# Performance work log

Measured on AMD Instinct MI355X. Metric: run time of the kernel, lower is better.

Reference implementation:

```python
import jax, jax.numpy as jnp
import numpy as np

B, N, D, EPG = 64, 1024, 128, 8192          # graphs, nodes/graph, feat dim, edges/graph
NTOT, ETOT = B * N, B * EPG
RATIO, LAMB, NEG = 0.8, 1.0, 0.2
K = int(np.ceil(RATIO * N))                  # 820 kept nodes per graph (static)


def setup_inputs() -> dict:
    key = jax.random.key(0)
    k1, k2, k3, k4, k5, k6 = jax.random.split(key, 6)
    feat = jax.random.normal(k1, (NTOT, D), jnp.float32)
    offs = (jnp.arange(B, dtype=jnp.int32) * N)[:, None]
    src = (jax.random.randint(k2, (B, EPG), 0, N, jnp.int32) + offs).reshape(-1)
    dst = (jax.random.randint(k3, (B, EPG), 0, N, jnp.int32) + offs).reshape(-1)
    e_feat = jnp.ones((ETOT,), jnp.float32)  # default e_feat=None -> ones
    # xavier-normal-ish params
    W = jax.random.normal(k4, (D, D), jnp.float32) * (2.0 / (D + D)) ** 0.5
    a = jax.random.normal(k5, (D, 1), jnp.float32) * (2.0 / (D + 1)) ** 0.5
    att = jax.random.normal(k6, (1, 2 * D), jnp.float32) * (2.0 / (1 + 2 * D)) ** 0.5
    return {"feat": feat, "e_feat": e_feat, "W": W, "a": a, "att": att,
            "src": src, "dst": dst}


def sparsemax(z, axis):
    """Dense sparsemax along `axis` (shift-invariant, same as edge_sparsemax
    per destination-node group after max subtraction)."""
    n = z.shape[axis]
    zs = -jnp.sort(-z, axis=axis)                      # descending
    cs = jnp.cumsum(zs, axis=axis)
    shp = [1] * z.ndim
    shp[axis] = n
    r = jnp.arange(1, n + 1, dtype=z.dtype).reshape(shp)
    supp = (1.0 + r * zs) > cs
    kz = supp.sum(axis=axis, keepdims=True)            # support size
    tau = (jnp.take_along_axis(cs, kz - 1, axis=axis) - 1.0) / kz.astype(z.dtype)
    return jnp.clip(z - tau, 0.0)


def reference(feat, e_feat, W, a, att, src, dst):
    # ---- NodeInfoScoreLayer (sym_norm=True) ----
    ones_e = jnp.ones_like(e_feat)
    out_deg = jax.ops.segment_sum(ones_e, src, NTOT)   # degrees incl. self loops
    in_deg = jax.ops.segment_sum(ones_e, dst, NTOT)
    sn = jnp.maximum(out_deg, 1.0) ** -0.5
    dn = jnp.maximum(in_deg, 1.0) ** -0.5
    nonself = (src != dst).astype(feat.dtype)          # remove_self_loop
    msg = (feat * sn[:, None])[src] * (e_feat * nonself)[:, None]   # u_mul_e
    agg = jax.ops.segment_sum(msg, dst, NTOT)                        # sum -> h
    info = jnp.abs(feat - agg * dn[:, None]).sum(axis=1)

    # ---- node attention gate ----
    attn = jax.nn.sigmoid(jax.nn.leaky_relu((feat @ W) @ a, 0.2).squeeze(-1))
    x_score = info * attn

    # ---- per-graph top-k (equal graph sizes -> static k) ----
    _, idx = jax.lax.top_k(x_score.reshape(B, N), K)
    perm = (idx + jnp.arange(B, dtype=idx.dtype)[:, None] * N).reshape(-1)
    feat_p = feat[perm]                                # [B*K, D]

    # ---- structure learning, sample=False path: per-graph dense blocks ----
    maskarr = jnp.full((NTOT,), -1, jnp.int32).at[perm].set(
        jnp.arange(B * K, dtype=jnp.int32))
    nr, nc = maskarr[src], maskarr[dst]
    valid = (nr >= 0) & (nc >= 0)                      # edges of pooled subgraph
    nr0 = jnp.where(valid, nr, 0)
    nc0 = jnp.where(valid, nc, 0)
    bb, ii, jj = nr0 // K, nr0 % K, nc0 % K            # block-diagonal coords

    fp = feat_p.reshape(B, K, D)
    wsrc = fp @ att[0, :D]                             # [B, K]
    wdst = fp @ att[0, D:]
    Wblk = jax.nn.leaky_relu(wsrc[:, :, None] + wdst[:, None, :], NEG)  # [B,K,K]
    Wblk = Wblk.at[bb, ii, jj].add(jnp.where(valid, LAMB * e_feat, 0.0))

    # edge_sparsemax: normalize over incoming edges of each dst node
    weights = sparsemax(Wblk, axis=1)                  # over src axis
    weights = jnp.where(jnp.abs(weights) > 1e-9, weights, 0.0)

    return feat_p, weights, perm, x_score
```

## Files before the change

kernel.cpp:

```cpp
#include <hip/hip_runtime.h>
#include <math.h>


static constexpr int B_    = 64;
static constexpr int N_    = 1024;
static constexpr int D_    = 128;
static constexpr int NTOT_ = B_ * N_;
static constexpr int ETOT_ = B_ * 8192;
static constexpr int K_    = 820;
static constexpr int BK_   = B_ * K_;
static constexpr float NEG_ = 0.2f;
static constexpr int CH_   = 128;
static constexpr int CPB_  = 7;
static constexpr int CAP_  = 64;
static constexpr int NSA_  = (NTOT_ + 2047) / 2048;
static constexpr int NSB_  = (BK_ + 2047) / 2048;
static constexpr int SFLAG = 0x40000000;

typedef float fvec4 __attribute__((ext_vector_type(4)));

__device__ __forceinline__ float lrelu(float x) { return x >= 0.f ? x : NEG_ * x; }

__global__ void k_deg_wa(const int* __restrict__ src, const int* __restrict__ dst,
                         int* __restrict__ outd, int* __restrict__ ind,
                         const float* __restrict__ W, const float* __restrict__ a,
                         float* __restrict__ waf) {
  int blk = blockIdx.x;
  if (blk < ETOT_ / 256) {
    int e = blk * 256 + threadIdx.x;
    atomicAdd(&outd[src[e]], 1);
    atomicAdd(&ind[dst[e]], 1);
  } else {
    int q = blk - ETOT_ / 256;
    int w = threadIdx.x >> 6, lane = threadIdx.x & 63;
    int wid = q * 4 + w;
    double a0 = (double)a[2 * lane], a1 = (double)a[2 * lane + 1];
#pragma unroll
    for (int r = 0; r < 4; ++r) {
      int d = wid * 4 + r;
      double s = (double)W[d * D_ + 2 * lane] * a0
               + (double)W[d * D_ + 2 * lane + 1] * a1;
#pragma unroll
      for (int off = 32; off > 0; off >>= 1) s += __shfl_down(s, off);
      if (lane == 0) waf[d] = (float)s;
    }
  }
}

__device__ __forceinline__ void scan2048(const int* __restrict__ in, int n, int blk,
                                         int nblk, int* __restrict__ partials,
                                         int* __restrict__ out) {
  int t = threadIdx.x;
  int w = t >> 6, lane = t & 63;
  int base = blk * 2048 + t * 4;
  int a0 = (base < n) ? in[base] : 0;
  int a1 = (base + 1 < n) ? in[base + 1] : 0;
  int a2 = (base + 2 < n) ? in[base + 2] : 0;
  int a3 = (base + 3 < n) ? in[base + 3] : 0;
  int s = a0 + a1 + a2 + a3;
  int inc = s;
#pragma unroll
  for (int off = 1; off < 64; off <<= 1) {
    int v = __shfl_up(inc, off);
    if (lane >= off) inc += v;
  }
  __shared__ int wtot[8];
  __shared__ int sbase;
  if (lane == 63) wtot[w] = inc;
  __syncthreads();
  if (t == 0) {
    int btot = 0;
#pragma unroll
    for (int q2 = 0; q2 < 8; ++q2) btot += wtot[q2];
    __hip_atomic_store(&partials[blk], btot | SFLAG, __ATOMIC_RELEASE,
                       __HIP_MEMORY_SCOPE_AGENT);
  }
  if (t < 64) {
    int v = 0;
    if (t < blk) {
      do {
        v = __hip_atomic_load(&partials[t], __ATOMIC_ACQUIRE,
                              __HIP_MEMORY_SCOPE_AGENT);
      } while (!(v & SFLAG));
      v &= ~SFLAG;
    }
#pragma unroll
    for (int off = 32; off > 0; off >>= 1) v += __shfl_down(v, off);
    if (t == 0) sbase = v;
  }
  __syncthreads();
  int wbase = 0;
  for (int q2 = 0; q2 < w; ++q2) wbase += wtot[q2];
  int ex = sbase + wbase + inc - s;
  if (base < n) out[base] = ex; ex += a0;
  if (base + 1 < n) out[base + 1] = ex; ex += a1;
  if (base + 2 < n) out[base + 2] = ex; ex += a2;
  if (base + 3 < n) out[base + 3] = ex; ex += a3;
  if (blk == nblk - 1 && t == 511) out[n] = ex;
}

__global__ void k_scanA(const int* __restrict__ in, int* __restrict__ partials,
                        int* __restrict__ out) {
  scan2048(in, NTOT_, blockIdx.x, NSA_, partials, out);
}

__global__ void k_fillcsr(const int* __restrict__ dst, const int* __restrict__ rowptr,
                          int* __restrict__ cursor, int* __restrict__ col) {
  int e = blockIdx.x * 256 + threadIdx.x;
  int v = dst[e];
  int p = atomicAdd(&cursor[v], 1);
  col[rowptr[v] + p] = e;
}

__global__ void k_agg(const float* __restrict__ feat, const float* __restrict__ e_feat,
                      const int* __restrict__ src, const int* __restrict__ col,
                      const int* __restrict__ rowptr, const int* __restrict__ outd,
                      const int* __restrict__ ind, const float* __restrict__ waf,
                      float* __restrict__ out_xs) {
  __shared__ int su[4][CAP_];
  __shared__ float ssc[4][CAP_];
  int g = blockIdx.x;
  int vb = (g & 7) * 2048 + (g >> 3);
  int w = threadIdx.x >> 6, lane = threadIdx.x & 63;
  int v = vb * 4 + w;
  int r0 = rowptr[v], r1 = rowptr[v + 1];
  int m = r1 - r0;
  int mm = m < CAP_ ? m : CAP_;
  for (int s = lane; s < mm; s += 64) {
    int e = col[r0 + s];
    int u = src[e];
    float sc = (u == v) ? 0.f : e_feat[e] / sqrtf(fmaxf((float)outd[u], 1.f));
    su[w][s] = u;
    ssc[w][s] = sc;
  }
  __syncthreads();
  const float2* f2 = (const float2*)feat;
  float2 f = f2[(size_t)v * 64 + lane];
  float ax = 0.f, ay = 0.f;
  int s = 0;
  for (; s + 4 <= mm; s += 4) {
    int u0 = su[w][s], u1 = su[w][s + 1], u2 = su[w][s + 2], u3 = su[w][s + 3];
    float c0 = ssc[w][s], c1 = ssc[w][s + 1], c2 = ssc[w][s + 2], c3 = ssc[w][s + 3];
    float2 f0 = f2[(size_t)u0 * 64 + lane];
    float2 f1 = f2[(size_t)u1 * 64 + lane];
    float2 fq = f2[(size_t)u2 * 64 + lane];
    float2 f3 = f2[(size_t)u3 * 64 + lane];
    ax += f0.x * c0 + f1.x * c1 + fq.x * c2 + f3.x * c3;
    ay += f0.y * c0 + f1.y * c1 + fq.y * c2 + f3.y * c3;
  }
  for (; s < mm; ++s) {
    float2 fu = f2[(size_t)su[w][s] * 64 + lane];
    ax += fu.x * ssc[w][s];
    ay += fu.y * ssc[w][s];
  }
  for (int sP = r0 + CAP_; sP < r1; ++sP) {
    int e = col[sP];
    int u = src[e];
    if (u == v) continue;
    float sc = e_feat[e] / sqrtf(fmaxf((float)outd[u], 1.f));
    float2 fu = f2[(size_t)u * 64 + lane];
    ax += fu.x * sc;
    ay += fu.y * sc;
  }
  float dn = 1.f / sqrtf(fmaxf((float)ind[v], 1.f));
  float info = fabsf(f.x - ax * dn) + fabsf(f.y - ay * dn);
  float dot = f.x * waf[2 * lane] + f.y * waf[2 * lane + 1];
#pragma unroll
  for (int off = 32; off > 0; off >>= 1) {
    info += __shfl_down(info, off);
    dot  += __shfl_down(dot, off);
  }
  if (lane == 0) {
    float sA = dot >= 0.f ? dot : 0.2f * dot;
    float attn = 1.f / (1.f + expf(-sA));
    out_xs[v] = info * attn;
  }
}

__global__ void k_topk(const float* __restrict__ xs, float* __restrict__ out_perm,
                       int* __restrict__ perm_i, int* __restrict__ maskarr) {
  __shared__ unsigned long long dv[1024];
  int b = blockIdx.x, t = threadIdx.x;
  for (int i = t; i < 1024; i += 512) {
    unsigned bits = __float_as_uint(xs[b * 1024 + i]);
    dv[i] = ((unsigned long long)bits << 32) | (unsigned)(N_ - 1 - i);
  }
  __syncthreads();
  for (int k2 = 2; k2 <= 1024; k2 <<= 1) {
    for (int j = k2 >> 1; j > 0; j >>= 1) {
      for (int i = t; i < 1024; i += 512) {
        int ixj = i ^ j;
        if (ixj > i) {
          unsigned long long a = dv[i], c = dv[ixj];
          bool dir = ((i & k2) == 0);
          if ((a > c) != dir) { dv[i] = c; dv[ixj] = a; }
        }
      }
      __syncthreads();
    }
  }
  for (int r = t; r < K_; r += 512) {
    int idx = N_ - 1 - (int)(dv[r] & 0xFFFFFFFFull);
    int node = b * N_ + idx;
    int pos = b * K_ + r;
    out_perm[pos] = (float)node;
    perm_i[pos] = node;
    maskarr[node] = pos;
  }
}

__global__ void k_gather_cnt2(const float* __restrict__ feat, const int* __restrict__ perm_i,
                              const float* __restrict__ att, float* __restrict__ out_featp,
                              float* __restrict__ wsrc, float* __restrict__ wdst,
                              const int* __restrict__ src, const int* __restrict__ dst,
                              const int* __restrict__ maskarr, int* __restrict__ cnt2) {
  int blk = blockIdx.x;
  if (blk < BK_ / 4) {
    int vb = (blk & 7) * 1640 + (blk >> 3);
    int gid = vb * 256 + threadIdx.x;
    int p = gid >> 6, lane = gid & 63;
    int node = perm_i[p];
    float2 f = ((const float2*)feat)[(size_t)node * 64 + lane];
    ((float2*)out_featp)[(size_t)p * 64 + lane] = f;
    float s1 = f.x * att[2 * lane] + f.y * att[2 * lane + 1];
    float s2 = f.x * att[D_ + 2 * lane] + f.y * att[D_ + 2 * lane + 1];
#pragma unroll
    for (int off = 32; off > 0; off >>= 1) {
      s1 += __shfl_down(s1, off);
      s2 += __shfl_down(s2, off);
    }
    if (lane == 0) { wsrc[p] = s1; wdst[p] = s2; }
  } else {
    int e = (blk - BK_ / 4) * 256 + threadIdx.x;
    int nr = maskarr[src[e]], nc = maskarr[dst[e]];
    if (nr >= 0 && nc >= 0) atomicAdd(&cnt2[nc], 1);
  }
}

__global__ void k_scanB_gsort(const int* __restrict__ cnt2, int* __restrict__ partials,
                              int* __restrict__ rowptr2, const float* __restrict__ wsrc,
                              float* __restrict__ ws_sorted, float* __restrict__ psum) {
  if (blockIdx.x < NSB_) {
    scan2048(cnt2, BK_, blockIdx.x, NSB_, partials, rowptr2);
    return;
  }
  __shared__ float sv[1024];
  __shared__ float sc[1024];
  int b = blockIdx.x - NSB_, t = threadIdx.x;
  for (int i = t; i < 1024; i += 512) sv[i] = (i < K_) ? wsrc[b * K_ + i] : -INFINITY;
  __syncthreads();
  for (int k2 = 2; k2 <= 1024; k2 <<= 1) {
    for (int j = k2 >> 1; j > 0; j >>= 1) {
      for (int i = t; i < 1024; i += 512) {
        int ixj = i ^ j;
        if (ixj > i) {
          float a = sv[i], c = sv[ixj];
          bool dir = ((i & k2) == 0);
          bool swapv = dir ? (c > a) : (a > c);
          if (swapv) { sv[i] = c; sv[ixj] = a; }
        }
      }
      __syncthreads();
    }
  }
  for (int i = t; i < 1024; i += 512) { ws_sorted[b * 1024 + i] = sv[i]; sc[i] = sv[i]; }
  __syncthreads();
  for (int off = 1; off < 1024; off <<= 1) {
    float tmp[2];
    for (int i = t, q = 0; i < 1024; i += 512, ++q) tmp[q] = (i >= off) ? sc[i - off] : 0.f;
    __syncthreads();
    for (int i = t, q = 0; i < 1024; i += 512, ++q) sc[i] += tmp[q];
    __syncthreads();
  }
  if (t == 0) psum[b * 1025] = 0.f;
  for (int i = t; i < 1024; i += 512) psum[b * 1025 + 1 + i] = sc[i];
}

__global__ void k_fill2(const int* __restrict__ src, const int* __restrict__ dst,
                        const int* __restrict__ maskarr, const float* __restrict__ e_feat,
                        const int* __restrict__ rowptr2, int* __restrict__ cursor2,
                        int* __restrict__ colii, float* __restrict__ colval) {
  int e = blockIdx.x * 256 + threadIdx.x;
  int nr = maskarr[src[e]], nc = maskarr[dst[e]];
  if (nr >= 0 && nc >= 0) {
    int p = atomicAdd(&cursor2[nc], 1);
    int s = rowptr2[nc] + p;
    colii[s] = nr;
    colval[s] = 1.0f * e_feat[e];
  }
}

__device__ __forceinline__ int cnt_gt_rng(const float* __restrict__ arr, float thr,
                                          int lo, int hi) {
  while (lo < hi) {
    int mid = (lo + hi) >> 1;
    if (arr[mid] > thr) lo = mid + 1; else hi = mid;
  }
  return lo;
}

__global__ void __launch_bounds__(128) k_tau(
    const float* __restrict__ wdst,
    const float* __restrict__ ws_sorted, const float* __restrict__ psum,
    const int* __restrict__ rowptr2, int* __restrict__ ucnt,
    int* __restrict__ colii, float* __restrict__ colval,
    const float* __restrict__ wsrc, float2* __restrict__ bval,
    float* __restrict__ tauv) {
  __shared__ float swss[1024];
  __shared__ float sps[1025];
  int b = blockIdx.x / CPB_;
  int chunk = blockIdx.x % CPB_;
  int t0 = threadIdx.x;
  for (int i = t0; i < 1024; i += 128) swss[i] = ws_sorted[b * 1024 + i];
  for (int i = t0; i < 1025; i += 128) sps[i] = psum[b * 1025 + i];
  __syncthreads();

  int j = chunk * CH_ + t0;
  if (j >= K_) return;
  int c = b * K_ + j;

  int r0 = rowptr2[c], r1 = rowptr2[c + 1];
  int wp = r0;
  for (int s = r0; s < r1; ++s) {
    int ii = colii[s];
    if (ii < 0) continue;
    float E = colval[s];
    for (int t2 = s + 1; t2 < r1; ++t2)
      if (colii[t2] == ii) { E += colval[t2]; colii[t2] = -1; }
    colii[wp] = ii; colval[wp] = E; ++wp;
  }
  int m = wp - r0;
  ucnt[c] = m;
  for (int s = r0; s < wp; ++s) bval[s] = make_float2(wsrc[colii[s]], colval[s]);

  float wd = wdst[c];
  int p = cnt_gt_rng(swss, -wd, 0, K_);
  float psp = sps[p];

  float mz = lrelu(swss[0] + wd);
  for (int s = 0; s < m; ++s) {
    float2 v = bval[r0 + s];
    mz = fmaxf(mz, lrelu(v.x + wd) + v.y);
  }

  float lo = mz - 1.0f, hi = mz;
  int nmin = 0, nmax = K_;
  for (int it = 0; it < 22; ++it) {
    float t = 0.5f * (lo + hi);
    float wthr = (t >= 0.f ? t : 5.f * t) - wd;
    int n = cnt_gt_rng(swss, wthr, nmin, nmax);
    float bsum = (n <= p) ? (sps[n] + n * wd)
                          : (psp + p * wd + NEG_ * (sps[n] - psp + (n - p) * wd));
    float g = bsum - n * t;
    for (int s = 0; s < m; ++s) {
      float2 v = bval[r0 + s];
      float bse = lrelu(v.x + wd);
      g += fmaxf(bse + v.y - t, 0.f) - fmaxf(bse - t, 0.f);
    }
    if (g > 1.f) { lo = t; nmax = n; } else { hi = t; nmin = n; }
  }
  float t = lo;
  float wthr = (t >= 0.f ? t : 5.f * t) - wd;
  int n = cnt_gt_rng(swss, wthr, nmin, nmax);
  float S = (n <= p) ? (sps[n] + n * wd)
                     : (psp + p * wd + NEG_ * (sps[n] - psp + (n - p) * wd));
  int cc = n;
  for (int s = 0; s < m; ++s) {
    float2 v = bval[r0 + s];
    float bse = lrelu(v.x + wd);
    float zz = bse + v.y;
    if (v.x > wthr) { S -= bse; cc -= 1; }
    if (zz > t)     { S += zz;  cc += 1; }
  }
  float tau = (cc < 1) ? (mz - 1.0f) : ((S - 1.0f) / (float)cc);
  tau = fminf(fmaxf(tau, mz - 1.0f), mz);
  tauv[c] = tau;
}

__global__ void k_dense4(const float* __restrict__ wsrc, const float* __restrict__ wdst,
                         const float* __restrict__ tauv, float* __restrict__ out_w) {
  int t = threadIdx.x;
  int j4 = t * 4;
  if (j4 >= K_) return;
  int r0 = blockIdx.x * 4;
  int b = r0 / K_;
  float4 wd = ((const float4*)(wdst + b * K_))[t];
  float4 ta = ((const float4*)(tauv + b * K_))[t];
  float4 ws4 = ((const float4*)wsrc)[blockIdx.x];
  const float wss[4] = {ws4.x, ws4.y, ws4.z, ws4.w};
#pragma unroll
  for (int q = 0; q < 4; ++q) {
    float ws = wss[q];
    fvec4 o;
    float z;
    z = lrelu(ws + wd.x) - ta.x; o.x = (z > 1e-9f) ? z : 0.f;
    z = lrelu(ws + wd.y) - ta.y; o.y = (z > 1e-9f) ? z : 0.f;
    z = lrelu(ws + wd.z) - ta.z; o.z = (z > 1e-9f) ? z : 0.f;
    z = lrelu(ws + wd.w) - ta.w; o.w = (z > 1e-9f) ? z : 0.f;
    __builtin_nontemporal_store(o, ((fvec4*)(out_w + (size_t)(r0 + q) * K_)) + t);
  }
}

__global__ void k_fix(const float* __restrict__ wsrc, const float* __restrict__ wdst,
                      const float* __restrict__ tauv, const int* __restrict__ rowptr2,
                      const int* __restrict__ ucnt, const int* __restrict__ colii,
                      const float* __restrict__ colval, float* __restrict__ out_w) {
  int c = blockIdx.x * 256 + threadIdx.x;
  int b = c / K_;
  int j = c - b * K_;
  float wd = wdst[c], ta = tauv[c];
  int r0 = rowptr2[c], m = ucnt[c];
  for (int s = 0; s < m; ++s) {
    int nr = colii[r0 + s];
    float z = lrelu(wsrc[nr] + wd) + colval[r0 + s];
    float v = z - ta;
    out_w[(size_t)nr * K_ + j] = (v > 1e-9f) ? v : 0.f;
  }
}

extern "C" void kernel_launch(void* const* d_in, const int* in_sizes, int n_in,
                              void* d_out, int out_size, void* d_ws, size_t ws_size,
                              hipStream_t stream) {
  const float* feat   = (const float*)d_in[0];
  const float* e_feat = (const float*)d_in[1];
  const float* W      = (const float*)d_in[2];
  const float* a      = (const float*)d_in[3];
  const float* att    = (const float*)d_in[4];
  const int*   src    = (const int*)d_in[5];
  const int*   dst    = (const int*)d_in[6];

  float* out_featp = (float*)d_out;
  float* out_w     = out_featp + (size_t)BK_ * D_;
  float* out_perm  = out_w + (size_t)BK_ * K_;
  float* out_xs    = out_perm + BK_;

  char* wsp = (char*)d_ws;
  auto carve = [&](size_t bytes) -> void* {
    void* pp = (void*)wsp;
    wsp += (bytes + 255) & ~(size_t)255;
    return pp;
  };
  float* waf       = (float*)carve((size_t)D_ * 4);
  float* wsrc      = (float*)carve((size_t)BK_ * 4);
  float* wdst      = (float*)carve((size_t)BK_ * 4);
  float* tauv      = (float*)carve((size_t)BK_ * 4);
  float* colval    = (float*)carve((size_t)ETOT_ * 4);
  float2* bval     = (float2*)carve((size_t)ETOT_ * 8);
  float* ws_sorted = (float*)carve((size_t)B_ * 1024 * 4);
  float* psum      = (float*)carve((size_t)B_ * 1025 * 4);
  int* rowptr      = (int*)carve((size_t)(NTOT_ + 1) * 4);
  int* rowptr2     = (int*)carve((size_t)(BK_ + 1) * 4);
  int* col         = (int*)carve((size_t)ETOT_ * 4);
  int* colii       = (int*)carve((size_t)ETOT_ * 4);
  int* perm_i      = (int*)carve((size_t)BK_ * 4);
  size_t zbytes    = ((size_t)NTOT_ * 3 + (size_t)BK_ * 2 + 64) * 4;
  int* zblk        = (int*)carve(zbytes);
  int* in_deg      = zblk;
  int* out_deg     = zblk + NTOT_;
  int* cursor      = zblk + 2 * NTOT_;
  int* cnt2        = zblk + 3 * NTOT_;
  int* cursor2     = cnt2 + BK_;
  int* partA       = cursor2 + BK_;
  int* partB       = partA + 32;
  int* maskarr     = (int*)carve((size_t)NTOT_ * 4);

  hipMemsetAsync(zblk, 0, zbytes, stream);
  hipMemsetAsync(maskarr, 0xFF, (size_t)NTOT_ * 4, stream);

  k_deg_wa<<<ETOT_ / 256 + 8, 256, 0, stream>>>(src, dst, out_deg, in_deg, W, a, waf);
  k_scanA<<<NSA_, 512, 0, stream>>>(in_deg, partA, rowptr);
  k_fillcsr<<<ETOT_ / 256, 256, 0, stream>>>(dst, rowptr, cursor, col);
  k_agg<<<NTOT_ / 4, 256, 0, stream>>>(feat, e_feat, src, col, rowptr, out_deg, in_deg,
                                       waf, out_xs);
  k_topk<<<B_, 512, 0, stream>>>(out_xs, out_perm, perm_i, maskarr);
  k_gather_cnt2<<<BK_ / 4 + ETOT_ / 256, 256, 0, stream>>>(
      feat, perm_i, att, out_featp, wsrc, wdst, src, dst, maskarr, cnt2);
  k_scanB_gsort<<<NSB_ + B_, 512, 0, stream>>>(cnt2, partB, rowptr2, wsrc,
                                               ws_sorted, psum);
  k_fill2<<<ETOT_ / 256, 256, 0, stream>>>(src, dst, maskarr, e_feat, rowptr2, cursor2,
                                           colii, colval);
  k_tau<<<B_ * CPB_, 128, 0, stream>>>(wdst, ws_sorted, psum, rowptr2, cursor2,
                                       colii, colval, wsrc, bval, tauv);
  k_dense4<<<BK_ / 4, 256, 0, stream>>>(wsrc, wdst, tauv, out_w);
  k_fix<<<BK_ / 256, 256, 0, stream>>>(wsrc, wdst, tauv, rowptr2, cursor2, colii, colval,
                                       out_w);
}
```

Before: 539.8 us.

## Fuse all stages into one cooperative persistent kernel with grid syncs

Replaces the chain of eleven kernel launches with a single cooperative kernel of 1024 blocks. Stages are separated by grid.sync() and each stage's work is strided across the fixed grid. This removes per-launch overhead and the gaps between kernels. In exchange, stages that need few blocks (top-k, the sorts) leave most of the grid idle while waiting at barriers. Block sizes also shrink from 512 to 256 threads in the sort and scan stages, which serialises more work per thread.

```diff
diff --git a/kernel.cpp b/kernel.cpp
--- a/kernel.cpp
+++ b/kernel.cpp
@@ -1,5 +1,8 @@
 #include <hip/hip_runtime.h>
+#include <hip/hip_cooperative_groups.h>
 #include <math.h>
+
+namespace cg = cooperative_groups;
 
 
 static constexpr int B_    = 64;
@@ -10,68 +13,46 @@
 static constexpr int K_    = 820;
 static constexpr int BK_   = B_ * K_;
 static constexpr float NEG_ = 0.2f;
-static constexpr int CH_   = 128;
-static constexpr int CPB_  = 7;
 static constexpr int CAP_  = 64;
 static constexpr int NSA_  = (NTOT_ + 2047) / 2048;
 static constexpr int NSB_  = (BK_ + 2047) / 2048;
 static constexpr int SFLAG = 0x40000000;
+static constexpr int GRID_ = 1024;
 
 typedef float fvec4 __attribute__((ext_vector_type(4)));
 
 __device__ __forceinline__ float lrelu(float x) { return x >= 0.f ? x : NEG_ * x; }
 
-__global__ void k_deg_wa(const int* __restrict__ src, const int* __restrict__ dst,
-                         int* __restrict__ outd, int* __restrict__ ind,
-                         const float* __restrict__ W, const float* __restrict__ a,
-                         float* __restrict__ waf) {
-  int blk = blockIdx.x;
-  if (blk < ETOT_ / 256) {
-    int e = blk * 256 + threadIdx.x;
-    atomicAdd(&outd[src[e]], 1);
-    atomicAdd(&ind[dst[e]], 1);
-  } else {
-    int q = blk - ETOT_ / 256;
-    int w = threadIdx.x >> 6, lane = threadIdx.x & 63;
-    int wid = q * 4 + w;
-    double a0 = (double)a[2 * lane], a1 = (double)a[2 * lane + 1];
-#pragma unroll
-    for (int r = 0; r < 4; ++r) {
-      int d = wid * 4 + r;
-      double s = (double)W[d * D_ + 2 * lane] * a0
-               + (double)W[d * D_ + 2 * lane + 1] * a1;
-#pragma unroll
-      for (int off = 32; off > 0; off >>= 1) s += __shfl_down(s, off);
-      if (lane == 0) waf[d] = (float)s;
-    }
-  }
+__device__ __forceinline__ int cnt_gt_rng(const float* __restrict__ arr, float thr,
+                                          int lo, int hi) {
+  while (lo < hi) {
+    int mid = (lo + hi) >> 1;
+    if (arr[mid] > thr) lo = mid + 1; else hi = mid;
+  }
+  return lo;
 }
 
-__device__ __forceinline__ void scan2048(const int* __restrict__ in, int n, int blk,
-                                         int nblk, int* __restrict__ partials,
-                                         int* __restrict__ out) {
-  int t = threadIdx.x;
-  int w = t >> 6, lane = t & 63;
-  int base = blk * 2048 + t * 4;
-  int a0 = (base < n) ? in[base] : 0;
-  int a1 = (base + 1 < n) ? in[base + 1] : 0;
-  int a2 = (base + 2 < n) ? in[base + 2] : 0;
-  int a3 = (base + 3 < n) ? in[base + 3] : 0;
-  int s = a0 + a1 + a2 + a3;
+__device__ __forceinline__ void scan2048c(const int* __restrict__ in, int n, int blk,
+                                          int nblk, int* __restrict__ partials,
+                                          int* __restrict__ out,
+                                          unsigned char* smem_) {
+  int t = threadIdx.x, w = t >> 6, lane = t & 63;
+  int* wtot = (int*)smem_;
+  int* sbasep = (int*)(smem_ + 16);
+  int base = blk * 2048 + t * 8;
+  int a[8], s = 0;
+#pragma unroll
+  for (int q = 0; q < 8; ++q) { a[q] = (base + q < n) ? in[base + q] : 0; s += a[q]; }
   int inc = s;
 #pragma unroll
   for (int off = 1; off < 64; off <<= 1) {
     int v = __shfl_up(inc, off);
     if (lane >= off) inc += v;
   }
-  __shared__ int wtot[8];
-  __shared__ int sbase;
   if (lane == 63) wtot[w] = inc;
   __syncthreads();
   if (t == 0) {
-    int btot = 0;
-#pragma unroll
-    for (int q2 = 0; q2 < 8; ++q2) btot += wtot[q2];
+    int btot = wtot[0] + wtot[1] + wtot[2] + wtot[3];
     __hip_atomic_store(&partials[blk], btot | SFLAG, __ATOMIC_RELEASE,
                        __HIP_MEMORY_SCOPE_AGENT);
   }
@@ -86,335 +67,342 @@
     }
 #pragma unroll
     for (int off = 32; off > 0; off >>= 1) v += __shfl_down(v, off);
-    if (t == 0) sbase = v;
+    if (t == 0) *sbasep = v;
   }
   __syncthreads();
   int wbase = 0;
-  for (int q2 = 0; q2 < w; ++q2) wbase += wtot[q2];
-  int ex = sbase + wbase + inc - s;
-  if (base < n) out[base] = ex; ex += a0;
-  if (base + 1 < n) out[base + 1] = ex; ex += a1;
-  if (base + 2 < n) out[base + 2] = ex; ex += a2;
-  if (base + 3 < n) out[base + 3] = ex; ex += a3;
-  if (blk == nblk - 1 && t == 511) out[n] = ex;
+  for (int q = 0; q < w; ++q) wbase += wtot[q];
+  int ex = *sbasep + wbase + inc - s;
+#pragma unroll
+  for (int q = 0; q < 8; ++q) { if (base + q < n) out[base + q] = ex; ex += a[q]; }
+  if (blk == nblk - 1 && t == 255) out[n] = ex;
 }
 
-__global__ void k_scanA(const int* __restrict__ in, int* __restrict__ partials,
-                        int* __restrict__ out) {
-  scan2048(in, NTOT_, blockIdx.x, NSA_, partials, out);
-}
-
-__global__ void k_fillcsr(const int* __restrict__ dst, const int* __restrict__ rowptr,
-                          int* __restrict__ cursor, int* __restrict__ col) {
-  int e = blockIdx.x * 256 + threadIdx.x;
-  int v = dst[e];
-  int p = atomicAdd(&cursor[v], 1);
-  col[rowptr[v] + p] = e;
-}
-
-__global__ void k_agg(const float* __restrict__ feat, const float* __restrict__ e_feat,
-                      const int* __restrict__ src, const int* __restrict__ col,
-                      const int* __restrict__ rowptr, const int* __restrict__ outd,
-                      const int* __restrict__ ind, const float* __restrict__ waf,
-                      float* __restrict__ out_xs) {
-  __shared__ int su[4][CAP_];
-  __shared__ float ssc[4][CAP_];
-  int g = blockIdx.x;
-  int vb = (g & 7) * 2048 + (g >> 3);
-  int w = threadIdx.x >> 6, lane = threadIdx.x & 63;
-  int v = vb * 4 + w;
-  int r0 = rowptr[v], r1 = rowptr[v + 1];
-  int m = r1 - r0;
-  int mm = m < CAP_ ? m : CAP_;
-  for (int s = lane; s < mm; s += 64) {
-    int e = col[r0 + s];
-    int u = src[e];
-    float sc = (u == v) ? 0.f : e_feat[e] / sqrtf(fmaxf((float)outd[u], 1.f));
-    su[w][s] = u;
-    ssc[w][s] = sc;
-  }
-  __syncthreads();
-  const float2* f2 = (const float2*)feat;
-  float2 f = f2[(size_t)v * 64 + lane];
-  float ax = 0.f, ay = 0.f;
-  int s = 0;
-  for (; s + 4 <= mm; s += 4) {
-    int u0 = su[w][s], u1 = su[w][s + 1], u2 = su[w][s + 2], u3 = su[w][s + 3];
-    float c0 = ssc[w][s], c1 = ssc[w][s + 1], c2 = ssc[w][s + 2], c3 = ssc[w][s + 3];
-    float2 f0 = f2[(size_t)u0 * 64 + lane];
-    float2 f1 = f2[(size_t)u1 * 64 + lane];
-    float2 fq = f2[(size_t)u2 * 64 + lane];
-    float2 f3 = f2[(size_t)u3 * 64 + lane];
-    ax += f0.x * c0 + f1.x * c1 + fq.x * c2 + f3.x * c3;
-    ay += f0.y * c0 + f1.y * c1 + fq.y * c2 + f3.y * c3;
-  }
-  for (; s < mm; ++s) {
-    float2 fu = f2[(size_t)su[w][s] * 64 + lane];
-    ax += fu.x * ssc[w][s];
-    ay += fu.y * ssc[w][s];
-  }
-  for (int sP = r0 + CAP_; sP < r1; ++sP) {
-    int e = col[sP];
-    int u = src[e];
-    if (u == v) continue;
-    float sc = e_feat[e] / sqrtf(fmaxf((float)outd[u], 1.f));
-    float2 fu = f2[(size_t)u * 64 + lane];
-    ax += fu.x * sc;
-    ay += fu.y * sc;
-  }
-  float dn = 1.f / sqrtf(fmaxf((float)ind[v], 1.f));
-  float info = fabsf(f.x - ax * dn) + fabsf(f.y - ay * dn);
-  float dot = f.x * waf[2 * lane] + f.y * waf[2 * lane + 1];
-#pragma unroll
-  for (int off = 32; off > 0; off >>= 1) {
-    info += __shfl_down(info, off);
-    dot  += __shfl_down(dot, off);
-  }
-  if (lane == 0) {
-    float sA = dot >= 0.f ? dot : 0.2f * dot;
-    float attn = 1.f / (1.f + expf(-sA));
-    out_xs[v] = info * attn;
-  }
-}
-
-__global__ void k_topk(const float* __restrict__ xs, float* __restrict__ out_perm,
-                       int* __restrict__ perm_i, int* __restrict__ maskarr) {
-  __shared__ unsigned long long dv[1024];
-  int b = blockIdx.x, t = threadIdx.x;
-  for (int i = t; i < 1024; i += 512) {
-    unsigned bits = __float_as_uint(xs[b * 1024 + i]);
-    dv[i] = ((unsigned long long)bits << 32) | (unsigned)(N_ - 1 - i);
-  }
-  __syncthreads();
-  for (int k2 = 2; k2 <= 1024; k2 <<= 1) {
-    for (int j = k2 >> 1; j > 0; j >>= 1) {
-      for (int i = t; i < 1024; i += 512) {
-        int ixj = i ^ j;
-        if (ixj > i) {
-          unsigned long long a = dv[i], c = dv[ixj];
-          bool dir = ((i & k2) == 0);
-          if ((a > c) != dir) { dv[i] = c; dv[ixj] = a; }
+struct MegaArgs {
+  const float* feat; const float* e_feat; const float* W; const float* a;
+  const float* att; const int* src; const int* dst;
+  float* out_featp; float* out_w; float* out_perm; float* out_xs;
+  float* waf; float* wsrc; float* wdst; float* tauv; float* colval;
+  float2* bval; float* ws_sorted; float* psum;
+  int* rowptr; int* rowptr2; int* col; int* colii; int* perm_i;
+  int* in_deg; int* out_deg; int* cursor; int* cnt2; int* cursor2;
+  int* partA; int* partB; int* maskarr;
+};
+
+__global__ void __launch_bounds__(256, 4) mega(MegaArgs A) {
+  cg::grid_group grid = cg::this_grid();
+  __shared__ __align__(16) unsigned char smem_[8448];
+  const int blk = blockIdx.x, t = threadIdx.x;
+  const int w = t >> 6, lane = t & 63;
+
+  for (int e = blk * 256 + t; e < ETOT_; e += GRID_ * 256) {
+    atomicAdd(&A.out_deg[A.src[e]], 1);
+    atomicAdd(&A.in_deg[A.dst[e]], 1);
+  }
+  if (blk < 8) {
+    int wid = blk * 4 + w;
+    double a0 = (double)A.a[2 * lane], a1 = (double)A.a[2 * lane + 1];
+#pragma unroll
+    for (int r = 0; r < 4; ++r) {
+      int d = wid * 4 + r;
+      double s = (double)A.W[d * D_ + 2 * lane] * a0
+               + (double)A.W[d * D_ + 2 * lane + 1] * a1;
+#pragma unroll
+      for (int off = 32; off > 0; off >>= 1) s += __shfl_down(s, off);
+      if (lane == 0) A.waf[d] = (float)s;
+    }
+  }
+  grid.sync();
+
+  if (blk < NSA_) scan2048c(A.in_deg, NTOT_, blk, NSA_, A.partA, A.rowptr, smem_);
+  grid.sync();
+
+  for (int e = blk * 256 + t; e < ETOT_; e += GRID_ * 256) {
+    int v = A.dst[e];
+    int p = atomicAdd(&A.cursor[v], 1);
+    A.col[A.rowptr[v] + p] = e;
+  }
+  grid.sync();
+
+  {
+    int* su = (int*)smem_;
+    float* ssc = (float*)(smem_ + 1024);
+    const float2* f2 = (const float2*)A.feat;
+    int x = blk & 7, idx = blk >> 3;
+    for (int pass = 0; pass < 16; ++pass) {
+      int v = x * 8192 + pass * 512 + idx * 4 + w;
+      int r0 = A.rowptr[v], r1 = A.rowptr[v + 1];
+      int m = r1 - r0;
+      int mm = m < CAP_ ? m : CAP_;
+      for (int s = lane; s < mm; s += 64) {
+        int e = A.col[r0 + s];
+        int u = A.src[e];
+        float sc = (u == v) ? 0.f : A.e_feat[e] / sqrtf(fmaxf((float)A.out_deg[u], 1.f));
+        su[w * CAP_ + s] = u;
+        ssc[w * CAP_ + s] = sc;
+      }
+      __syncthreads();
+      float2 f = f2[(size_t)v * 64 + lane];
+      float ax = 0.f, ay = 0.f;
+      int s = 0;
+      for (; s + 4 <= mm; s += 4) {
+        int u0 = su[w * CAP_ + s], u1 = su[w * CAP_ + s + 1];
+        int u2 = su[w * CAP_ + s + 2], u3 = su[w * CAP_ + s + 3];
+        float c0 = ssc[w * CAP_ + s], c1 = ssc[w * CAP_ + s + 1];
+        float c2 = ssc[w * CAP_ + s + 2], c3 = ssc[w * CAP_ + s + 3];
+        float2 f0 = f2[(size_t)u0 * 64 + lane];
+        float2 f1 = f2[(size_t)u1 * 64 + lane];
+        float2 fq = f2[(size_t)u2 * 64 + lane];
+        float2 f3 = f2[(size_t)u3 * 64 + lane];
+        ax += f0.x * c0 + f1.x * c1 + fq.x * c2 + f3.x * c3;
+        ay += f0.y * c0 + f1.y * c1 + fq.y * c2 + f3.y * c3;
+      }
+      for (; s < mm; ++s) {
+        float2 fu = f2[(size_t)su[w * CAP_ + s] * 64 + lane];
+        ax += fu.x * ssc[w * CAP_ + s];
+        ay += fu.y * ssc[w * CAP_ + s];
+      }
+      for (int sP = r0 + CAP_; sP < r1; ++sP) {
+        int e = A.col[sP];
+        int u = A.src[e];
+        if (u == v) continue;
+        float sc = A.e_feat[e] / sqrtf(fmaxf((float)A.out_deg[u], 1.f));
+        float2 fu = f2[(size_t)u * 64 + lane];
+        ax += fu.x * sc;
+        ay += fu.y * sc;
+      }
+      float dn = 1.f / sqrtf(fmaxf((float)A.in_deg[v], 1.f));
+      float info = fabsf(f.x - ax * dn) + fabsf(f.y - ay * dn);
+      float dot = f.x * A.waf[2 * lane] + f.y * A.waf[2 * lane + 1];
+#pragma unroll
+      for (int off = 32; off > 0; off >>= 1) {
+        info += __shfl_down(info, off);
+        dot  += __shfl_down(dot, off);
+      }
+      if (lane == 0) {
+        float sA = dot >= 0.f ? dot : 0.2f * dot;
+        float attn = 1.f / (1.f + expf(-sA));
+        A.out_xs[v] = info * attn;
+      }
+      __syncthreads();
+    }
+  }
+  grid.sync();
+
+  if (blk < B_) {
+    unsigned long long* dv = (unsigned long long*)smem_;
+    for (int i = t; i < 1024; i += 256) {
+      unsigned bits = __float_as_uint(A.out_xs[blk * 1024 + i]);
+      dv[i] = ((unsigned long long)bits << 32) | (unsigned)(N_ - 1 - i);
+    }
+    __syncthreads();
+    for (int k2 = 2; k2 <= 1024; k2 <<= 1) {
+      for (int j = k2 >> 1; j > 0; j >>= 1) {
+        for (int i = t; i < 1024; i += 256) {
+          int ixj = i ^ j;
+          if (ixj > i) {
+            unsigned long long a = dv[i], c = dv[ixj];
+            bool dir = ((i & k2) == 0);
+            if ((a > c) != dir) { dv[i] = c; dv[ixj] = a; }
+          }
         }
-      }
+        __syncthreads();
+      }
+    }
+    for (int r = t; r < K_; r += 256) {
+      int idx = N_ - 1 - (int)(dv[r] & 0xFFFFFFFFull);
+      int node = blk * N_ + idx;
+      int pos = blk * K_ + r;
+      A.out_perm[pos] = (float)node;
+      A.perm_i[pos] = node;
+      A.maskarr[node] = pos;
+    }
+  }
+  grid.sync();
+
+  {
+    int x = blk & 7, bi = blk >> 3;
+    const float2* f2 = (const float2*)A.feat;
+    for (int pass = 0; pass < 13; ++pass) {
+      int off = pass * 512 + bi * 4 + w;
+      if (off < 6560) {
+        int p = x * 6560 + off;
+        int node = A.perm_i[p];
+        float2 f = f2[(size_t)node * 64 + lane];
+        ((float2*)A.out_featp)[(size_t)p * 64 + lane] = f;
+        float s1 = f.x * A.att[2 * lane] + f.y * A.att[2 * lane + 1];
+        float s2 = f.x * A.att[D_ + 2 * lane] + f.y * A.att[D_ + 2 * lane + 1];
+#pragma unroll
+        for (int o2 = 32; o2 > 0; o2 >>= 1) {
+          s1 += __shfl_down(s1, o2);
+          s2 += __shfl_down(s2, o2);
+        }
+        if (lane == 0) { A.wsrc[p] = s1; A.wdst[p] = s2; }
+      }
+    }
+    for (int e = blk * 256 + t; e < ETOT_; e += GRID_ * 256) {
+      int nr = A.maskarr[A.src[e]], nc = A.maskarr[A.dst[e]];
+      if (nr >= 0 && nc >= 0) atomicAdd(&A.cnt2[nc], 1);
+    }
+  }
+  grid.sync();
+
+  if (blk < NSB_) {
+    scan2048c(A.cnt2, BK_, blk, NSB_, A.partB, A.rowptr2, smem_);
+  } else if (blk >= 32 && blk < 32 + B_) {
+    float* sv = (float*)smem_;
+    float* sc = (float*)(smem_ + 4096);
+    int b = blk - 32;
+    for (int i = t; i < 1024; i += 256) sv[i] = (i < K_) ? A.wsrc[b * K_ + i] : -INFINITY;
+    __syncthreads();
+    for (int k2 = 2; k2 <= 1024; k2 <<= 1) {
+      for (int j = k2 >> 1; j > 0; j >>= 1) {
+        for (int i = t; i < 1024; i += 256) {
+          int ixj = i ^ j;
+          if (ixj > i) {
+            float a = sv[i], c = sv[ixj];
+            bool dir = ((i & k2) == 0);
+            bool swapv = dir ? (c > a) : (a > c);
+            if (swapv) { sv[i] = c; sv[ixj] = a; }
+          }
+        }
+        __syncthreads();
+      }
+    }
+    for (int i = t; i < 1024; i += 256) { A.ws_sorted[b * 1024 + i] = sv[i]; sc[i] = sv[i]; }
+    __syncthreads();
+    for (int off = 1; off < 1024; off <<= 1) {
+      float tmp[4];
+      for (int i = t, q = 0; i < 1024; i += 256, ++q) tmp[q] = (i >= off) ? sc[i - off] : 0.f;
       __syncthreads();
-    }
-  }
-  for (int r = t; r < K_; r += 512) {
-    int idx = N_ - 1 - (int)(dv[r] & 0xFFFFFFFFull);
-    int node = b * N_ + idx;
-    int pos = b * K_ + r;
-    out_perm[pos] = (float)node;
-    perm_i[pos] = node;
-    maskarr[node] = pos;
-  }
-}
-
-__global__ void k_gather_cnt2(const float* __restrict__ feat, const int* __restrict__ perm_i,
-                              const float* __restrict__ att, float* __restrict__ out_featp,
-                              float* __restrict__ wsrc, float* __restrict__ wdst,
-                              const int* __restrict__ src, const int* __restrict__ dst,
-                              const int* __restrict__ maskarr, int* __restrict__ cnt2) {
-  int blk = blockIdx.x;
-  if (blk < BK_ / 4) {
-    int vb = (blk & 7) * 1640 + (blk >> 3);
-    int gid = vb * 256 + threadIdx.x;
-    int p = gid >> 6, lane = gid & 63;
-    int node = perm_i[p];
-    float2 f = ((const float2*)feat)[(size_t)node * 64 + lane];
-    ((float2*)out_featp)[(size_t)p * 64 + lane] = f;
-    float s1 = f.x * att[2 * lane] + f.y * att[2 * lane + 1];
-    float s2 = f.x * att[D_ + 2 * lane] + f.y * att[D_ + 2 * lane + 1];
-#pragma unroll
-    for (int off = 32; off > 0; off >>= 1) {
-      s1 += __shfl_down(s1, off);
-      s2 += __shfl_down(s2, off);
-    }
-    if (lane == 0) { wsrc[p] = s1; wdst[p] = s2; }
-  } else {
-    int e = (blk - BK_ / 4) * 256 + threadIdx.x;
-    int nr = maskarr[src[e]], nc = maskarr[dst[e]];
-    if (nr >= 0 && nc >= 0) atomicAdd(&cnt2[nc], 1);
-  }
-}
-
-__global__ void k_scanB_gsort(const int* __restrict__ cnt2, int* __restrict__ partials,
-                              int* __restrict__ rowptr2, const float* __restrict__ wsrc,
-                              float* __restrict__ ws_sorted, float* __restrict__ psum) {
-  if (blockIdx.x < NSB_) {
-    scan2048(cnt2, BK_, blockIdx.x, NSB_, partials, rowptr2);
-    return;
-  }
-  __shared__ float sv[1024];
-  __shared__ float sc[1024];
-  int b = blockIdx.x - NSB_, t = threadIdx.x;
-  for (int i = t; i < 1024; i += 512) sv[i] = (i < K_) ? wsrc[b * K_ + i] : -INFINITY;
-  __syncthreads();
-  for (int k2 = 2; k2 <= 1024; k2 <<= 1) {
-    for (int j = k2 >> 1; j > 0; j >>= 1) {
-      for (int i = t; i < 1024; i += 512) {
-        int ixj = i ^ j;
-        if (ixj > i) {
-          float a = sv[i], c = sv[ixj];
-          bool dir = ((i & k2) == 0);
-          bool swapv = dir ? (c > a) : (a > c);
-          if (swapv) { sv[i] = c; sv[ixj] = a; }
+      for (int i = t, q = 0; i < 1024; i += 256, ++q) sc[i] += tmp[q];
+      __syncthreads();
+    }
+    if (t == 0) A.psum[b * 1025] = 0.f;
+    for (int i = t; i < 1024; i += 256) A.psum[b * 1025 + 1 + i] = sc[i];
+  }
+  grid.sync();
+
+  for (int e = blk * 256 + t; e < ETOT_; e += GRID_ * 256) {
+    int nr = A.maskarr[A.src[e]], nc = A.maskarr[A.dst[e]];
+    if (nr >= 0 && nc >= 0) {
+      int p = atomicAdd(&A.cursor2[nc], 1);
+      int s = A.rowptr2[nc] + p;
+      A.colii[s] = nr;
+      A.colval[s] = 1.0f * A.e_feat[e];
+    }
+  }
+  grid.sync();
+
+  if (blk < 256) {
+    float* swss = (float*)smem_;
+    float* sps = (float*)(smem_ + 4096);
+    int b = blk >> 2, chunk = blk & 3;
+    for (int i = t; i < 1024; i += 256) swss[i] = A.ws_sorted[b * 1024 + i];
+    for (int i = t; i < 1025; i += 256) sps[i] = A.psum[b * 1025 + i];
+    __syncthreads();
+    if (t < 205) {
+      int j = chunk * 205 + t;
+      int c = b * K_ + j;
+
+      int r0 = A.rowptr2[c], r1 = A.rowptr2[c + 1];
+      int wp = r0;
+      for (int s = r0; s < r1; ++s) {
+        int ii = A.colii[s];
+        if (ii < 0) continue;
+        float E = A.colval[s];
+        for (int t2 = s + 1; t2 < r1; ++t2)
+          if (A.colii[t2] == ii) { E += A.colval[t2]; A.colii[t2] = -1; }
+        A.colii[wp] = ii; A.colval[wp] = E; ++wp;
+      }
+      int m = wp - r0;
+      A.cursor2[c] = m;
+      for (int s = r0; s < wp; ++s)
+        A.bval[s] = make_float2(A.wsrc[A.colii[s]], A.colval[s]);
+
+      float wd = A.wdst[c];
+      int p = cnt_gt_rng(swss, -wd, 0, K_);
+      float psp = sps[p];
+
+      float mz = lrelu(swss[0] + wd);
+      for (int s = 0; s < m; ++s) {
+        float2 v = A.bval[r0 + s];
+        mz = fmaxf(mz, lrelu(v.x + wd) + v.y);
+      }
+
+      float lo = mz - 1.0f, hi = mz;
+      int nmin = 0, nmax = K_;
+      for (int it = 0; it < 22; ++it) {
+        float tt = 0.5f * (lo + hi);
+        float wthr = (tt >= 0.f ? tt : 5.f * tt) - wd;
+        int n = cnt_gt_rng(swss, wthr, nmin, nmax);
+        float bsum = (n <= p) ? (sps[n] + n * wd)
+                              : (psp + p * wd + NEG_ * (sps[n] - psp + (n - p) * wd));
+        float g = bsum - n * tt;
+        for (int s = 0; s < m; ++s) {
+          float2 v = A.bval[r0 + s];
+          float bse = lrelu(v.x + wd);
+          g += fmaxf(bse + v.y - tt, 0.f) - fmaxf(bse - tt, 0.f);
         }
-      }
-      __syncthreads();
-    }
-  }
-  for (int i = t; i < 1024; i += 512) { ws_sorted[b * 1024 + i] = sv[i]; sc[i] = sv[i]; }
-  __syncthreads();
-  for (int off = 1; off < 1024; off <<= 1) {
-    float tmp[2];
-    for (int i = t, q = 0; i < 1024; i += 512, ++q) tmp[q] = (i >= off) ? sc[i - off] : 0.f;
-    __syncthreads();
-    for (int i = t, q = 0; i < 1024; i += 512, ++q) sc[i] += tmp[q];
-    __syncthreads();
-  }
-  if (t == 0) psum[b * 1025] = 0.f;
-  for (int i = t; i < 1024; i += 512) psum[b * 1025 + 1 + i] = sc[i];
-}
-
-__global__ void k_fill2(const int* __restrict__ src, const int* __restrict__ dst,
-                        const int* __restrict__ maskarr, const float* __restrict__ e_feat,
-                        const int* __restrict__ rowptr2, int* __restrict__ cursor2,
-                        int* __restrict__ colii, float* __restrict__ colval) {
-  int e = blockIdx.x * 256 + threadIdx.x;
-  int nr = maskarr[src[e]], nc = maskarr[dst[e]];
-  if (nr >= 0 && nc >= 0) {
-    int p = atomicAdd(&cursor2[nc], 1);
-    int s = rowptr2[nc] + p;
-    colii[s] = nr;
-    colval[s] = 1.0f * e_feat[e];
-  }
-}
-
-__device__ __forceinline__ int cnt_gt_rng(const float* __restrict__ arr, float thr,
-                                          int lo, int hi) {
-  while (lo < hi) {
-    int mid = (lo + hi) >> 1;
-    if (arr[mid] > thr) lo = mid + 1; else hi = mid;
-  }
-  return lo;
-}
-
-__global__ void __launch_bounds__(128) k_tau(
-    const float* __restrict__ wdst,
-    const float* __restrict__ ws_sorted, const float* __restrict__ psum,
-    const int* __restrict__ rowptr2, int* __restrict__ ucnt,
-    int* __restrict__ colii, float* __restrict__ colval,
-    const float* __restrict__ wsrc, float2* __restrict__ bval,
-    float* __restrict__ tauv) {
-  __shared__ float swss[1024];
-  __shared__ float sps[1025];
-  int b = blockIdx.x / CPB_;
-  int chunk = blockIdx.x % CPB_;
-  int t0 = threadIdx.x;
-  for (int i = t0; i < 1024; i += 128) swss[i] = ws_sorted[b * 1024 + i];
-  for (int i = t0; i < 1025; i += 128) sps[i] = psum[b * 1025 + i];
-  __syncthreads();
-
-  int j = chunk * CH_ + t0;
-  if (j >= K_) return;
-  int c = b * K_ + j;
-
-  int r0 = rowptr2[c], r1 = rowptr2[c + 1];
-  int wp = r0;
-  for (int s = r0; s < r1; ++s) {
-    int ii = colii[s];
-    if (ii < 0) continue;
-    float E = colval[s];
-    for (int t2 = s + 1; t2 < r1; ++t2)
-      if (colii[t2] == ii) { E += colval[t2]; colii[t2] = -1; }
-    colii[wp] = ii; colval[wp] = E; ++wp;
-  }
-  int m = wp - r0;
-  ucnt[c] = m;
-  for (int s = r0; s < wp; ++s) bval[s] = make_float2(wsrc[colii[s]], colval[s]);
-
-  float wd = wdst[c];
-  int p = cnt_gt_rng(swss, -wd, 0, K_);
-  float psp = sps[p];
-
-  float mz = lrelu(swss[0] + wd);
-  for (int s = 0; s < m; ++s) {
-    float2 v = bval[r0 + s];
-    mz = fmaxf(mz, lrelu(v.x + wd) + v.y);
-  }
-
-  float lo = mz - 1.0f, hi = mz;
-  int nmin = 0, nmax = K_;
-  for (int it = 0; it < 22; ++it) {
-    float t = 0.5f * (lo + hi);
-    float wthr = (t >= 0.f ? t : 5.f * t) - wd;
-    int n = cnt_gt_rng(swss, wthr, nmin, nmax);
-    float bsum = (n <= p) ? (sps[n] + n * wd)
-                          : (psp + p * wd + NEG_ * (sps[n] - psp + (n - p) * wd));
-    float g = bsum - n * t;
-    for (int s = 0; s < m; ++s) {
-      float2 v = bval[r0 + s];
-      float bse = lrelu(v.x + wd);
-      g += fmaxf(bse + v.y - t, 0.f) - fmaxf(bse - t, 0.f);
-    }
-    if (g > 1.f) { lo = t; nmax = n; } else { hi = t; nmin = n; }
-  }
-  float t = lo;
-  float wthr = (t >= 0.f ? t : 5.f * t) - wd;
-  int n = cnt_gt_rng(swss, wthr, nmin, nmax);
-  float S = (n <= p) ? (sps[n] + n * wd)
-                     : (psp + p * wd + NEG_ * (sps[n] - psp + (n - p) * wd));
-  int cc = n;
-  for (int s = 0; s < m; ++s) {
-    float2 v = bval[r0 + s];
-    float bse = lrelu(v.x + wd);
-    float zz = bse + v.y;
-    if (v.x > wthr) { S -= bse; cc -= 1; }
-    if (zz > t)     { S += zz;  cc += 1; }
-  }
-  float tau = (cc < 1) ? (mz - 1.0f) : ((S - 1.0f) / (float)cc);
-  tau = fminf(fmaxf(tau, mz - 1.0f), mz);
-  tauv[c] = tau;
-}
-
-__global__ void k_dense4(const float* __restrict__ wsrc, const float* __restrict__ wdst,
-                         const float* __restrict__ tauv, float* __restrict__ out_w) {
-  int t = threadIdx.x;
-  int j4 = t * 4;
-  if (j4 >= K_) return;
-  int r0 = blockIdx.x * 4;
-  int b = r0 / K_;
-  float4 wd = ((const float4*)(wdst + b * K_))[t];
-  float4 ta = ((const float4*)(tauv + b * K_))[t];
-  float4 ws4 = ((const float4*)wsrc)[blockIdx.x];
-  const float wss[4] = {ws4.x, ws4.y, ws4.z, ws4.w};
-#pragma unroll
-  for (int q = 0; q < 4; ++q) {
-    float ws = wss[q];
-    fvec4 o;
-    float z;
-    z = lrelu(ws + wd.x) - ta.x; o.x = (z > 1e-9f) ? z : 0.f;
-    z = lrelu(ws + wd.y) - ta.y; o.y = (z > 1e-9f) ? z : 0.f;
-    z = lrelu(ws + wd.z) - ta.z; o.z = (z > 1e-9f) ? z : 0.f;
-    z = lrelu(ws + wd.w) - ta.w; o.w = (z > 1e-9f) ? z : 0.f;
-    __builtin_nontemporal_store(o, ((fvec4*)(out_w + (size_t)(r0 + q) * K_)) + t);
-  }
-}
-
-__global__ void k_fix(const float* __restrict__ wsrc, const float* __restrict__ wdst,
-                      const float* __restrict__ tauv, const int* __restrict__ rowptr2,
-                      const int* __restrict__ ucnt, const int* __restrict__ colii,
-                      const float* __restrict__ colval, float* __restrict__ out_w) {
-  int c = blockIdx.x * 256 + threadIdx.x;
-  int b = c / K_;
-  int j = c - b * K_;
-  float wd = wdst[c], ta = tauv[c];
-  int r0 = rowptr2[c], m = ucnt[c];
-  for (int s = 0; s < m; ++s) {
-    int nr = colii[r0 + s];
-    float z = lrelu(wsrc[nr] + wd) + colval[r0 + s];
-    float v = z - ta;
-    out_w[(size_t)nr * K_ + j] = (v > 1e-9f) ? v : 0.f;
+        if (g > 1.f) { lo = tt; nmax = n; } else { hi = tt; nmin = n; }
+      }
+      float tt = lo;
+      float wthr = (tt >= 0.f ? tt : 5.f * tt) - wd;
+      int n = cnt_gt_rng(swss, wthr, nmin, nmax);
+      float S = (n <= p) ? (sps[n] + n * wd)
+                         : (psp + p * wd + NEG_ * (sps[n] - psp + (n - p) * wd));
+      int cc = n;
+      for (int s = 0; s < m; ++s) {
+        float2 v = A.bval[r0 + s];
+        float bse = lrelu(v.x + wd);
+        float zz = bse + v.y;
+        if (v.x > wthr) { S -= bse; cc -= 1; }
+        if (zz > tt)    { S += zz;  cc += 1; }
+      }
+      float tau = (cc < 1) ? (mz - 1.0f) : ((S - 1.0f) / (float)cc);
+      tau = fminf(fmaxf(tau, mz - 1.0f), mz);
+      A.tauv[c] = tau;
+    }
+  }
+  grid.sync();
+
+  for (int q4 = blk; q4 < BK_ / 4; q4 += GRID_) {
+    if (t < 205) {
+      int r0 = q4 * 4;
+      int b = r0 / K_;
+      float4 wd = ((const float4*)(A.wdst + b * K_))[t];
+      float4 ta = ((const float4*)(A.tauv + b * K_))[t];
+      float4 ws4 = ((const float4*)A.wsrc)[q4];
+      const float wss[4] = {ws4.x, ws4.y, ws4.z, ws4.w};
+#pragma unroll
+      for (int q = 0; q < 4; ++q) {
+        float ws = wss[q];
+        fvec4 o;
+        float z;
+        z = lrelu(ws + wd.x) - ta.x; o.x = (z > 1e-9f) ? z : 0.f;
+        z = lrelu(ws + wd.y) - ta.y; o.y = (z > 1e-9f) ? z : 0.f;
+        z = lrelu(ws + wd.z) - ta.z; o.z = (z > 1e-9f) ? z : 0.f;
+        z = lrelu(ws + wd.w) - ta.w; o.w = (z > 1e-9f) ? z : 0.f;
+        __builtin_nontemporal_store(o, ((fvec4*)(A.out_w + (size_t)(r0 + q) * K_)) + t);
+      }
+    }
+  }
+  grid.sync();
+
+  {
+    int c = blk * 256 + t;
+    if (c < BK_) {
+      int b = c / K_;
+      int j = c - b * K_;
+      float wd = A.wdst[c], ta = A.tauv[c];
+      int r0 = A.rowptr2[c], m = A.cursor2[c];
+      for (int s = 0; s < m; ++s) {
+        int nr = A.colii[r0 + s];
+        float z = lrelu(A.wsrc[nr] + wd) + A.colval[r0 + s];
+        float v = z - ta;
+        A.out_w[(size_t)nr * K_ + j] = (v > 1e-9f) ? v : 0.f;
+      }
+    }
   }
 }
 
@@ -464,24 +452,21 @@
   int* partB       = partA + 32;
   int* maskarr     = (int*)carve((size_t)NTOT_ * 4);
 
-  hipMemsetAsync(zblk, 0, zbytes, stream);
-  hipMemsetAsync(maskarr, 0xFF, (size_t)NTOT_ * 4, stream);
-
-  k_deg_wa<<<ETOT_ / 256 + 8, 256, 0, stream>>>(src, dst, out_deg, in_deg, W, a, waf);
-  k_scanA<<<NSA_, 512, 0, stream>>>(in_deg, partA, rowptr);
-  k_fillcsr<<<ETOT_ / 256, 256, 0, stream>>>(dst, rowptr, cursor, col);
-  k_agg<<<NTOT_ / 4, 256, 0, stream>>>(feat, e_feat, src, col, rowptr, out_deg, in_deg,
-                                       waf, out_xs);
-  k_topk<<<B_, 512, 0, stream>>>(out_xs, out_perm, perm_i, maskarr);
-  k_gather_cnt2<<<BK_ / 4 + ETOT_ / 256, 256, 0, stream>>>(
-      feat, perm_i, att, out_featp, wsrc, wdst, src, dst, maskarr, cnt2);
-  k_scanB_gsort<<<NSB_ + B_, 512, 0, stream>>>(cnt2, partB, rowptr2, wsrc,
-                                               ws_sorted, psum);
-  k_fill2<<<ETOT_ / 256, 256, 0, stream>>>(src, dst, maskarr, e_feat, rowptr2, cursor2,
-                                           colii, colval);
-  k_tau<<<B_ * CPB_, 128, 0, stream>>>(wdst, ws_sorted, psum, rowptr2, cursor2,
-                                       colii, colval, wsrc, bval, tauv);
-  k_dense4<<<BK_ / 4, 256, 0, stream>>>(wsrc, wdst, tauv, out_w);
-  k_fix<<<BK_ / 256, 256, 0, stream>>>(wsrc, wdst, tauv, rowptr2, cursor2, colii, colval,
-                                       out_w);
+  (void)hipMemsetAsync(zblk, 0, zbytes, stream);
+  (void)hipMemsetAsync(maskarr, 0xFF, (size_t)NTOT_ * 4, stream);
+
+  MegaArgs ma;
+  ma.feat = feat; ma.e_feat = e_feat; ma.W = W; ma.a = a; ma.att = att;
+  ma.src = src; ma.dst = dst;
+  ma.out_featp = out_featp; ma.out_w = out_w; ma.out_perm = out_perm;
+  ma.out_xs = out_xs;
+  ma.waf = waf; ma.wsrc = wsrc; ma.wdst = wdst; ma.tauv = tauv;
+  ma.colval = colval; ma.bval = bval; ma.ws_sorted = ws_sorted; ma.psum = psum;
+  ma.rowptr = rowptr; ma.rowptr2 = rowptr2; ma.col = col; ma.colii = colii;
+  ma.perm_i = perm_i;
+  ma.in_deg = in_deg; ma.out_deg = out_deg; ma.cursor = cursor; ma.cnt2 = cnt2;
+  ma.cursor2 = cursor2; ma.partA = partA; ma.partB = partB; ma.maskarr = maskarr;
+
+  void* kargs[] = { &ma };
+  (void)hipLaunchCooperativeKernel(mega, dim3(GRID_), dim3(256), kargs, 0, stream);
 }
```

New measurement: 1.738 ms. 222% more time.
